# Kernel tuning notes

Measured on AMD Instinct MI355X. Metric: run time of the kernel, lower is better.

## Reference

```python
import jax, jax.numpy as jnp
import numpy as np

N_EMBD = 1024
N_HEAD = 16
HEAD_DIM = N_EMBD // N_HEAD  # 64
R = 8
D_STD = HEAD_DIM - R         # 56
BLOCK_SIZE = 2048
B, T = 2, 2048
NEG = -1e9


def setup_inputs() -> dict:
    key = jax.random.key(0)
    ks = jax.random.split(key, 8)
    x = jax.random.normal(ks[0], (B, T, N_EMBD), dtype=jnp.float32)
    Wqkv = jax.random.normal(ks[1], (3 * N_EMBD, N_EMBD), dtype=jnp.float32) * 0.02
    Wproj = jax.random.normal(ks[2], (N_EMBD, N_EMBD), dtype=jnp.float32) * 0.02
    W_recip = jax.random.normal(ks[3], (HEAD_DIM, R), dtype=jnp.float32) * 0.02
    # mixing weights must be positive (sqrt is taken); match init scale
    w_std = jnp.full((N_HEAD,), 0.5, dtype=jnp.float32)
    w_rec = jnp.full((N_HEAD,), 0.3, dtype=jnp.float32)  # > threshold -> all heads RA
    w_disc = jnp.full((N_HEAD,), 0.2, dtype=jnp.float32)
    d_bias = jax.random.normal(ks[4], (N_HEAD, BLOCK_SIZE), dtype=jnp.float32) * 0.02
    return {"x": x, "Wqkv": Wqkv, "Wproj": Wproj, "W_recip": W_recip,
            "w_std": w_std, "w_rec": w_rec, "w_disc": w_disc, "d_bias": d_bias}


def reference(x, Wqkv, Wproj, W_recip, w_std, w_rec, w_disc, d_bias):
    Bx, Tx, C = x.shape
    H, hd = N_HEAD, HEAD_DIM
    qkv = x @ Wqkv.T                                   # (B,T,3C)
    q, k, v = jnp.split(qkv, 3, axis=-1)
    def heads(t):
        return t.reshape(Bx, Tx, H, hd).transpose(0, 2, 1, 3)  # (B,H,T,hd)
    q, k, v = heads(q), heads(k), heads(v)
    q_low = jnp.einsum('bhtd,dr->bhtr', q, W_recip)    # (B,H,T,R)
    k_low = jnp.einsum('bhtd,dr->bhtr', k, W_recip)
    sw_std = jnp.sqrt(w_std)[None, :, None, None]
    sw_rec = jnp.sqrt(w_rec)[None, :, None, None]
    # cross augmentation: q side carries k_low, k side carries q_low
    q_aug = jnp.concatenate([sw_std * q[..., :D_STD], sw_rec * k_low], axis=-1)
    k_aug = jnp.concatenate([sw_std * k[..., :D_STD], sw_rec * q_low], axis=-1)
    scale = 1.0 / jnp.sqrt(jnp.asarray(hd, dtype=x.dtype))
    scores = jnp.einsum('bhqd,bhkd->bhqk', q_aug, k_aug) * scale
    # per-head learned bias over key positions, broadcast over queries
    bias = w_disc[None, :, None, None] * d_bias[:, :Tx][None, :, None, :]
    scores = scores + bias
    causal = jnp.tril(jnp.ones((Tx, Tx), dtype=bool))
    scores = jnp.where(causal[None, None], scores, NEG)
    attn = jax.nn.softmax(scores, axis=-1)
    out = jnp.einsum('bhqk,bhkd->bhqd', attn, v)       # (B,H,T,hd)
    out = out.transpose(0, 2, 1, 3).reshape(Bx, Tx, C)
    return out @ Wproj.T
```

## Files before the change

kernel.cpp:

```cpp
#include <hip/hip_runtime.h>
#include <math.h>

#define T_SEQ 2048
#define NH 16
#define HD 64
#define CEMB 1024
#define NEGINF -3.0e38f
#define LOG2E 1.4426950408889634f

typedef unsigned short ushort;
typedef unsigned int uint;
typedef __attribute__((ext_vector_type(8))) short short8;
typedef __attribute__((ext_vector_type(4))) float f32x4;

#if __has_builtin(__builtin_amdgcn_exp2f)
#define EXP2(x) __builtin_amdgcn_exp2f(x)
#else
#define EXP2(x) exp2f(x)
#endif

__device__ __forceinline__ float b2f(ushort h) {
    union { uint u; float f; } cv; cv.u = ((uint)h) << 16; return cv.f;
}
__device__ __forceinline__ ushort f2b(float f) {
    union { float f; uint u; } cv; cv.f = f;
    return (ushort)((cv.u + 0x7FFF + ((cv.u >> 16) & 1)) >> 16);
}
__device__ __forceinline__ ushort f2b_fast(float f) {
    union { float f; uint u; } cv; cv.f = f;
    return (ushort)((cv.u + 0x8000) >> 16);
}
__device__ __forceinline__ uint pack_bf16(float a, float b) {
    union { float f; uint u; } ua, ub; ua.f = a; ub.f = b;
    return __builtin_amdgcn_perm(ub.u + 0x8000u, ua.u + 0x8000u, 0x07060302u);
}
__device__ __forceinline__ void gl2lds16(const ushort* g, ushort* l) {
    __builtin_amdgcn_global_load_lds(
        (const __attribute__((address_space(1))) void*)g,
        (__attribute__((address_space(3))) void*)l, 16, 0, 0);
}

__global__ __launch_bounds__(256) void prep_kernel(
    const float* __restrict__ x, const float* __restrict__ Wqkv,
    const float* __restrict__ Wproj, const float* __restrict__ W_recip,
    const float* __restrict__ w_disc, const float* __restrict__ d_bias,
    ushort* __restrict__ xb, ushort* __restrict__ wqkvb,
    ushort* __restrict__ wprojb, float* __restrict__ bias_pre)
{
    const int bid = blockIdx.x;
    if (bid < 8192) {
        const float* src; ushort* dst; int off;
        if (bid < 4096)      { src = x;     dst = xb;     off = bid; }
        else if (bid < 7168) { src = Wqkv;  dst = wqkvb;  off = bid - 4096; }
        else                 { src = Wproj; dst = wprojb; off = bid - 7168; }
        const int i = (off * 256 + threadIdx.x) * 4;
        const float4 v = *(const float4*)&src[i];
        ushort4 o;
        o.x = f2b(v.x); o.y = f2b(v.y); o.z = f2b(v.z); o.w = f2b(v.w);
        *(ushort4*)&dst[i] = o;
        return;
    }
    if (bid >= 8224) {
        const int h = bid - 8224;
        const float wd = w_disc[h] * LOG2E;
        const int j = h * T_SEQ + threadIdx.x * 8;
        const float4 a = *(const float4*)&d_bias[j];
        const float4 c = *(const float4*)&d_bias[j + 4];
        float4 oa, oc;
        oa.x = a.x * wd; oa.y = a.y * wd; oa.z = a.z * wd; oa.w = a.w * wd;
        oc.x = c.x * wd; oc.y = c.y * wd; oc.z = c.z * wd; oc.w = c.w * wd;
        *(float4*)&bias_pre[j] = oa;
        *(float4*)&bias_pre[j + 4] = oc;
        return;
    }
    const int wb = bid - 8192;
    const int qk = wb >> 4, h = wb & 15;
    const int e0 = threadIdx.x * 4;
    f32x4 acc[8];
    #pragma unroll
    for (int r = 0; r < 8; ++r) acc[r] = (f32x4){0.f, 0.f, 0.f, 0.f};
    #pragma unroll 4
    for (int d = 0; d < 64; ++d) {
        const float4 xv = *(const float4*)&Wqkv[(size_t)(qk * 1024 + h * 64 + d) * 1024 + e0];
        #pragma unroll
        for (int r = 0; r < 8; ++r) {
            const float w = W_recip[d * 8 + r];
            acc[r][0] = fmaf(w, xv.x, acc[r][0]);
            acc[r][1] = fmaf(w, xv.y, acc[r][1]);
            acc[r][2] = fmaf(w, xv.z, acc[r][2]);
            acc[r][3] = fmaf(w, xv.w, acc[r][3]);
        }
    }
    #pragma unroll
    for (int r = 0; r < 8; ++r) {
        ushort4 o;
        o.x = f2b(acc[r][0]); o.y = f2b(acc[r][1]);
        o.z = f2b(acc[r][2]); o.w = f2b(acc[r][3]);
        *(ushort4*)&wqkvb[(size_t)(3072 + qk * 128 + h * 8 + r) * 1024 + e0] = o;
    }
}

#define GEMM_CORE(Aptr, Bptr, KDIM, SMEMN)                                     \
    __shared__ __align__(16) ushort SMEM[SMEMN];                               \
    ushort* const Asl = SMEM;                                                  \
    ushort* const Bsl = SMEM + 8192;                                           \
    const int row0 = blockIdx.x * 128;                                         \
    const int col0 = blockIdx.y * 128;                                         \
    const int tid = threadIdx.x;                                               \
    const int wave = tid >> 6, lane = tid & 63;                                \
    const int wm = wave >> 1, wn = wave & 1;                                   \
    const int quad = lane >> 4, lq = lane & 15;                                \
    const int l7 = lq & 7;                                                     \
    f32x4 acc[4][4];                                                           \
    _Pragma("unroll") for (int i = 0; i < 4; ++i)                              \
        _Pragma("unroll") for (int j = 0; j < 4; ++j)                          \
            acc[i][j] = (f32x4){0.f, 0.f, 0.f, 0.f};                           \
    for (int k0 = 0; k0 < (KDIM); k0 += 64) {                                  \
        _Pragma("unroll") for (int p = 0; p < 4; ++p) {                        \
            const int idx = p * 256 + tid;                                     \
            const int row = idx >> 3, slot = idx & 7;                          \
            const int kc = (slot ^ (row & 7)) << 3;                            \
            gl2lds16(&(Aptr)[(size_t)(row0 + row) * (KDIM) + k0 + kc], &Asl[idx * 8]); \
            gl2lds16(&(Bptr)[(size_t)(col0 + row) * (KDIM) + k0 + kc], &Bsl[idx * 8]); \
        }                                                                      \
        __syncthreads();                                                       \
        _Pragma("unroll") for (int ks = 0; ks < 2; ++ks) {                     \
            short8 af[4], bf[4];                                               \
            _Pragma("unroll") for (int i = 0; i < 4; ++i)                      \
                af[i] = *(const short8*)&Asl[(wm * 64 + i * 16 + lq) * 64 +    \
                                             (((ks * 4 + quad) ^ l7) << 3)];   \
            _Pragma("unroll") for (int j = 0; j < 4; ++j)                      \
                bf[j] = *(const short8*)&Bsl[(wn * 64 + j * 16 + lq) * 64 +    \
                                             (((ks * 4 + quad) ^ l7) << 3)];   \
            _Pragma("unroll") for (int i = 0; i < 4; ++i)                      \
                _Pragma("unroll") for (int j = 0; j < 4; ++j)                  \
                    acc[i][j] = __builtin_amdgcn_mfma_f32_16x16x32_bf16(       \
                        af[i], bf[j], acc[i][j], 0, 0, 0);                     \
        }                                                                      \
        __syncthreads();                                                       \
    }

__global__ __launch_bounds__(256, 4) void gemm_qkv_kernel(
    const ushort* __restrict__ A, const ushort* __restrict__ Bt,
    const float* __restrict__ w_std, const float* __restrict__ w_rec,
    ushort* __restrict__ qh, ushort* __restrict__ kh, ushort* __restrict__ vt)
{
    GEMM_CORE(A, Bt, 1024, 128 * 136)
    ushort* const Cs = SMEM;

    if (col0 >= 2048 && col0 < 3072) {
        #pragma unroll
        for (int j = 0; j < 4; ++j) {
            const int cc = col0 + wn * 64 + j * 16 + lq;
            const int h = (cc >> 6) & 15;
            const int d = cc & 63;
            #pragma unroll
            for (int i = 0; i < 4; ++i) {
                const int rr0 = row0 + wm * 64 + i * 16 + quad * 4;
                const int b = rr0 >> 11, t0 = rr0 & 2047;
                ushort4 pv;
                pv.x = f2b(acc[i][j][0]); pv.y = f2b(acc[i][j][1]);
                pv.z = f2b(acc[i][j][2]); pv.w = f2b(acc[i][j][3]);
                *(ushort4*)&vt[((((size_t)b * NH + h) * HD + d) * T_SEQ + t0)] = pv;
            }
        }
    } else if (col0 < 2048) {
        const bool isq = (col0 < 1024);
        #pragma unroll
        for (int j = 0; j < 4; ++j) {
            const int colc = wn * 64 + j * 16 + lq;
            const int h = ((col0 + colc) >> 6) & 15;
            const float sc = isq ? w_std[h] * (0.125f * LOG2E) : 1.0f;
            #pragma unroll
            for (int i = 0; i < 4; ++i)
                #pragma unroll
                for (int r = 0; r < 4; ++r)
                    Cs[(wm * 64 + i * 16 + quad * 4 + r) * 136 + colc] =
                        f2b(acc[i][j][r] * sc);
        }
        __syncthreads();
        ushort* dst = isq ? qh : kh;
        const int hbase = (col0 >> 6) & 15;
        #pragma unroll
        for (int rep = 0; rep < 8; ++rep) {
            const int id = rep * 256 + tid;
            const int row = id >> 4, chunk = id & 15;
            if ((chunk & 7) == 7) continue;
            const int h = hbase + (chunk >> 3);
            const int d = (chunk & 7) * 8;
            const int rr = row0 + row;
            const int b = rr >> 11, t = rr & 2047;
            const uint4 val = *(const uint4*)&Cs[row * 136 + chunk * 8];
            *(uint4*)&dst[((((size_t)b * NH + h) * T_SEQ + t) * HD + d)] = val;
        }
    } else {
        const bool isqlow = (col0 < 3200);
        #pragma unroll
        for (int j = 0; j < 4; ++j) {
            const int colc = wn * 64 + j * 16 + lq;
            const int h = colc >> 3;
            const float sc = isqlow ? 1.0f : w_rec[h] * (0.125f * LOG2E);
            #pragma unroll
            for (int i = 0; i < 4; ++i)
                #pragma unroll
                for (int r = 0; r < 4; ++r)
                    Cs[(wm * 64 + i * 16 + quad * 4 + r) * 136 + colc] =
                        f2b(acc[i][j][r] * sc);
        }
        __syncthreads();
        ushort* dst = isqlow ? kh : qh;
        #pragma unroll
        for (int rep = 0; rep < 8; ++rep) {
            const int id = rep * 256 + tid;
            const int row = id >> 4, h = id & 15;
            const int rr = row0 + row;
            const int b = rr >> 11, t = rr & 2047;
            const uint4 val = *(const uint4*)&Cs[row * 136 + h * 8];
            *(uint4*)&dst[((((size_t)b * NH + h) * T_SEQ + t) * HD + 56)] = val;
        }
    }
}

__global__ __launch_bounds__(256, 4) void gemm_proj_kernel(
    const ushort* __restrict__ A, const ushort* __restrict__ Bt,
    float* __restrict__ C)
{
    GEMM_CORE(A, Bt, 1024, 16384)
    #pragma unroll
    for (int i = 0; i < 4; ++i) {
        #pragma unroll
        for (int r = 0; r < 4; ++r) {
            const int rr = row0 + wm * 64 + i * 16 + quad * 4 + r;
            #pragma unroll
            for (int j = 0; j < 4; ++j) {
                const int cc = col0 + wn * 64 + j * 16 + lq;
                C[(size_t)rr * 1024 + cc] = acc[i][j][r];
            }
        }
    }
}

__global__ __launch_bounds__(256, 4) void attn_kernel(
    const ushort* __restrict__ qa, const ushort* __restrict__ ka,
    const ushort* __restrict__ vt, const float* __restrict__ bias_pre,
    ushort* __restrict__ out)
{
    __shared__ __align__(16) ushort Qs[64 * 64];
    __shared__ __align__(16) ushort KPs[128 * 64];
    __shared__ __align__(16) ushort Vs[64 * 128];
    const int bh = blockIdx.x;
    const int qt = 31 - blockIdx.y;
    const int h = bh & 15;
    const int b = bh >> 4;
    const int tid = threadIdx.x;
    const int wave = tid >> 6, lane = tid & 63;
    const int quad = lane >> 4, lq = lane & 15;
    const int l7 = lq & 7;
    const size_t base = (size_t)bh * T_SEQ * HD;

    #pragma unroll
    for (int rep = 0; rep < 2; ++rep) {
        const int idx = rep * 256 + tid;
        const int row = idx >> 3, slot = idx & 7;
        gl2lds16(&qa[base + (size_t)(qt * 64 + row) * 64 + ((slot ^ (row & 7)) << 3)],
                 &Qs[idx * 8]);
    }
    __syncthreads();
    short8 bq[2];
    #pragma unroll
    for (int ks = 0; ks < 2; ++ks)
        bq[ks] = *(const short8*)&Qs[(wave * 16 + lq) * 64 + (((ks * 4 + quad) ^ l7) << 3)];

    f32x4 o4[4];
    #pragma unroll
    for (int dt = 0; dt < 4; ++dt) o4[dt] = (f32x4){0.f, 0.f, 0.f, 0.f};
    float lsum = 0.f;
    const int qrow = qt * 64 + wave * 16 + lq;
    const int prow = (wave * 16 + lq) * 128;
    const int nchunks = (qt + 2) >> 1;
    const float* bias_h = &bias_pre[h * T_SEQ];

    for (int c = 0; c < nchunks; ++c) {
        const int k0 = c * 128;
        if (c) __syncthreads();
        #pragma unroll
        for (int rep = 0; rep < 4; ++rep) {
            const int idx = rep * 256 + tid;
            const int row = idx >> 3, slot = idx & 7;
            gl2lds16(&ka[base + (size_t)(k0 + row) * 64 + ((slot ^ (row & 7)) << 3)],
                     &KPs[idx * 8]);
        }
        #pragma unroll
        for (int rep = 0; rep < 4; ++rep) {
            const int idx = rep * 256 + tid;
            const int row = idx >> 4, slot = idx & 15;
            gl2lds16(&vt[base + (size_t)row * T_SEQ + k0 + ((slot ^ (row & 15)) << 3)],
                     &Vs[idx * 8]);
        }
        __syncthreads();

        f32x4 s4[8];
        #pragma unroll
        for (int nt = 0; nt < 8; ++nt)
            s4[nt] = *(const f32x4*)&bias_h[k0 + nt * 16 + quad * 4];
        #pragma unroll
        for (int ks = 0; ks < 2; ++ks)
            #pragma unroll
            for (int nt = 0; nt < 8; ++nt) {
                const short8 ak = *(const short8*)
                    &KPs[(nt * 16 + lq) * 64 + (((ks * 4 + quad) ^ l7) << 3)];
                s4[nt] = __builtin_amdgcn_mfma_f32_16x16x32_bf16(
                    ak, bq[ks], s4[nt], 0, 0, 0);
            }
        __syncthreads();

        const bool lastc = (c == nchunks - 1);
        #pragma unroll
        for (int nt = 0; nt < 8; ++nt) {
            f32x4 sv = s4[nt];
            if (lastc) {
                const int kb = k0 + nt * 16 + quad * 4;
                #pragma unroll
                for (int r = 0; r < 4; ++r)
                    if (kb + r > qrow) sv[r] = NEGINF;
            }
            const float p0 = EXP2(sv[0]), p1 = EXP2(sv[1]);
            const float p2 = EXP2(sv[2]), p3 = EXP2(sv[3]);
            lsum += (p0 + p1) + (p2 + p3);
            const int pcol = (nt * 16 + quad * 4) ^ (l7 << 3);
            uint2 pv; pv.x = pack_bf16(p0, p1); pv.y = pack_bf16(p2, p3);
            *(uint2*)&KPs[prow + pcol] = pv;
        }

        #pragma unroll
        for (int ks = 0; ks < 4; ++ks) {
            const short8 bp = *(const short8*)
                &KPs[prow + ((ks * 32 + quad * 8) ^ (l7 << 3))];
            #pragma unroll
            for (int dt = 0; dt < 4; ++dt) {
                const short8 av = *(const short8*)
                    &Vs[(dt * 16 + lq) * 128 + (((ks * 4 + quad) ^ lq) << 3)];
                o4[dt] = __builtin_amdgcn_mfma_f32_16x16x32_bf16(
                    av, bp, o4[dt], 0, 0, 0);
            }
        }
    }

    lsum += __shfl_xor(lsum, 16, 64);
    lsum += __shfl_xor(lsum, 32, 64);
    const float inv = 1.0f / lsum;
    const size_t obase = ((size_t)b * T_SEQ + qrow) * CEMB + h * HD;
    #pragma unroll
    for (int dt = 0; dt < 4; ++dt) {
        ushort4 ov;
        ov.x = f2b_fast(o4[dt][0] * inv);
        ov.y = f2b_fast(o4[dt][1] * inv);
        ov.z = f2b_fast(o4[dt][2] * inv);
        ov.w = f2b_fast(o4[dt][3] * inv);
        *(ushort4*)&out[obase + dt * 16 + quad * 4] = ov;
    }
}

extern "C" void kernel_launch(void* const* d_in, const int* in_sizes, int n_in,
                              void* d_out, int out_size, void* d_ws, size_t ws_size,
                              hipStream_t stream) {
    const float* x       = (const float*)d_in[0];
    const float* Wqkv    = (const float*)d_in[1];
    const float* Wproj   = (const float*)d_in[2];
    const float* W_recip = (const float*)d_in[3];
    const float* w_std   = (const float*)d_in[4];
    const float* w_rec   = (const float*)d_in[5];
    const float* w_disc  = (const float*)d_in[6];
    const float* d_bias  = (const float*)d_in[7];
    float* out = (float*)d_out;

    const size_t NX = (size_t)4096 * 1024;
    const size_t NWQKVX = (size_t)3328 * 1024;
    const size_t NWPROJ = (size_t)1024 * 1024;
    ushort* xb     = (ushort*)d_ws;
    ushort* wqkvb  = xb + NX;
    ushort* wprojb = wqkvb + NWQKVX;
    ushort* qh     = wprojb + NWPROJ;
    ushort* kh     = qh + NX;
    ushort* vt     = kh + NX;
    ushort* ao     = vt + NX;
    float*  bias_pre = (float*)(ao + NX);

    prep_kernel<<<8240, 256, 0, stream>>>(x, Wqkv, Wproj, W_recip, w_disc, d_bias,
                                          xb, wqkvb, wprojb, bias_pre);
    gemm_qkv_kernel<<<dim3(32, 26), 256, 0, stream>>>(xb, wqkvb, w_std, w_rec, qh, kh, vt);
    attn_kernel<<<dim3(32, 32), 256, 0, stream>>>(qh, kh, vt, bias_pre, ao);
    gemm_proj_kernel<<<dim3(32, 8), 256, 0, stream>>>(ao, wprojb, out);
}
```

Measured before the change: 191.8 us.

## Pair light and heavy causal query tiles per block, sharing K/V loads

Each attention block now handles two query tiles, qt and 31-qt, so causal work is balanced across blocks and each K/V chunk loaded into LDS serves both tiles. P gets its own LDS buffer so the barrier between score computation and the P writes can go, and the last diagonal chunk skips its empty half when the tile index is even. The grid is halved and launch bounds drop to 2 blocks per CU because of the extra registers and LDS, which lowers occupancy.

```diff
diff --git a/kernel.cpp b/kernel.cpp
--- a/kernel.cpp
+++ b/kernel.cpp
@@ -240,18 +240,54 @@
     }
 }
 
-__global__ __launch_bounds__(256, 4) void attn_kernel(
+#define TILE_COMPUTE(bq, o4, lsum, qrow, NTL) do {                            \
+    f32x4 s4[8];                                                              \
+    _Pragma("unroll") for (int nt = 0; nt < (NTL); ++nt)                      \
+        s4[nt] = *(const f32x4*)&bias_h[k0 + nt * 16 + quad * 4];             \
+    _Pragma("unroll") for (int ks = 0; ks < 2; ++ks)                          \
+        _Pragma("unroll") for (int nt = 0; nt < (NTL); ++nt) {                \
+            const short8 ak = *(const short8*)                                \
+                &Ks[(nt * 16 + lq) * 64 + (((ks * 4 + quad) ^ l7) << 3)];     \
+            s4[nt] = __builtin_amdgcn_mfma_f32_16x16x32_bf16(                 \
+                ak, (bq)[ks], s4[nt], 0, 0, 0);                               \
+        }                                                                     \
+    _Pragma("unroll") for (int nt = 0; nt < (NTL); ++nt) {                    \
+        f32x4 sv = s4[nt];                                                    \
+        const int kb = k0 + nt * 16 + quad * 4;                               \
+        _Pragma("unroll") for (int r = 0; r < 4; ++r)                         \
+            if (kb + r > (qrow)) sv[r] = NEGINF;                              \
+        const float p0 = EXP2(sv[0]), p1 = EXP2(sv[1]);                       \
+        const float p2 = EXP2(sv[2]), p3 = EXP2(sv[3]);                       \
+        (lsum) += (p0 + p1) + (p2 + p3);                                      \
+        const int pcol = (nt * 16 + quad * 4) ^ (l7 << 3);                    \
+        uint2 pv; pv.x = pack_bf16(p0, p1); pv.y = pack_bf16(p2, p3);         \
+        *(uint2*)&Ps[prow + pcol] = pv;                                       \
+    }                                                                         \
+    _Pragma("unroll") for (int ks = 0; ks < (NTL) / 2; ++ks) {                \
+        const short8 bp = *(const short8*)                                    \
+            &Ps[prow + ((ks * 32 + quad * 8) ^ (l7 << 3))];                   \
+        _Pragma("unroll") for (int dt = 0; dt < 4; ++dt) {                    \
+            const short8 av = *(const short8*)                                \
+                &Vs[(dt * 16 + lq) * 128 + (((ks * 4 + quad) ^ lq) << 3)];    \
+            (o4)[dt] = __builtin_amdgcn_mfma_f32_16x16x32_bf16(               \
+                av, bp, (o4)[dt], 0, 0, 0);                                   \
+        }                                                                     \
+    }                                                                         \
+} while (0)
+
+__global__ __launch_bounds__(256, 2) void attn_kernel(
     const ushort* __restrict__ qa, const ushort* __restrict__ ka,
     const ushort* __restrict__ vt, const float* __restrict__ bias_pre,
     ushort* __restrict__ out)
 {
-    __shared__ __align__(16) ushort Qs[64 * 64];
-    __shared__ __align__(16) ushort KPs[128 * 64];
+    __shared__ __align__(16) ushort Qs[2 * 64 * 64];
+    __shared__ __align__(16) ushort Ks[128 * 64];
+    __shared__ __align__(16) ushort Ps[64 * 128];
     __shared__ __align__(16) ushort Vs[64 * 128];
     const int bh = blockIdx.x;
-    const int qt = 31 - blockIdx.y;
-    const int h = bh & 15;
-    const int b = bh >> 4;
+    const int qtA = blockIdx.y;
+    const int qtB = 31 - blockIdx.y;
+    const int h = bh & 15, b = bh >> 4;
     const int tid = threadIdx.x;
     const int wave = tid >> 6, lane = tid & 63;
     const int quad = lane >> 4, lq = lane & 15;
@@ -262,25 +298,33 @@
     for (int rep = 0; rep < 2; ++rep) {
         const int idx = rep * 256 + tid;
         const int row = idx >> 3, slot = idx & 7;
-        gl2lds16(&qa[base + (size_t)(qt * 64 + row) * 64 + ((slot ^ (row & 7)) << 3)],
-                 &Qs[idx * 8]);
+        const int kc = (slot ^ (row & 7)) << 3;
+        gl2lds16(&qa[base + (size_t)(qtA * 64 + row) * 64 + kc], &Qs[idx * 8]);
+        gl2lds16(&qa[base + (size_t)(qtB * 64 + row) * 64 + kc], &Qs[4096 + idx * 8]);
     }
     __syncthreads();
-    short8 bq[2];
-    #pragma unroll
-    for (int ks = 0; ks < 2; ++ks)
-        bq[ks] = *(const short8*)&Qs[(wave * 16 + lq) * 64 + (((ks * 4 + quad) ^ l7) << 3)];
-
-    f32x4 o4[4];
-    #pragma unroll
-    for (int dt = 0; dt < 4; ++dt) o4[dt] = (f32x4){0.f, 0.f, 0.f, 0.f};
-    float lsum = 0.f;
-    const int qrow = qt * 64 + wave * 16 + lq;
+    short8 bqA[2], bqB[2];
+    #pragma unroll
+    for (int ks = 0; ks < 2; ++ks) {
+        const int off = (wave * 16 + lq) * 64 + (((ks * 4 + quad) ^ l7) << 3);
+        bqA[ks] = *(const short8*)&Qs[off];
+        bqB[ks] = *(const short8*)&Qs[4096 + off];
+    }
+
+    f32x4 o4A[4], o4B[4];
+    #pragma unroll
+    for (int dt = 0; dt < 4; ++dt) {
+        o4A[dt] = (f32x4){0.f, 0.f, 0.f, 0.f};
+        o4B[dt] = (f32x4){0.f, 0.f, 0.f, 0.f};
+    }
+    float lsumA = 0.f, lsumB = 0.f;
+    const int qrowA = qtA * 64 + wave * 16 + lq;
+    const int qrowB = qtB * 64 + wave * 16 + lq;
     const int prow = (wave * 16 + lq) * 128;
-    const int nchunks = (qt + 2) >> 1;
+    const int nA = (qtA + 2) >> 1, nB = (qtB + 2) >> 1;
     const float* bias_h = &bias_pre[h * T_SEQ];
 
-    for (int c = 0; c < nchunks; ++c) {
+    for (int c = 0; c < nB; ++c) {
         const int k0 = c * 128;
         if (c) __syncthreads();
         #pragma unroll
@@ -288,7 +332,7 @@
             const int idx = rep * 256 + tid;
             const int row = idx >> 3, slot = idx & 7;
             gl2lds16(&ka[base + (size_t)(k0 + row) * 64 + ((slot ^ (row & 7)) << 3)],
-                     &KPs[idx * 8]);
+                     &Ks[idx * 8]);
         }
         #pragma unroll
         for (int rep = 0; rep < 4; ++rep) {
@@ -299,65 +343,35 @@
         }
         __syncthreads();
 
-        f32x4 s4[8];
-        #pragma unroll
-        for (int nt = 0; nt < 8; ++nt)
-            s4[nt] = *(const f32x4*)&bias_h[k0 + nt * 16 + quad * 4];
-        #pragma unroll
-        for (int ks = 0; ks < 2; ++ks)
-            #pragma unroll
-            for (int nt = 0; nt < 8; ++nt) {
-                const short8 ak = *(const short8*)
-                    &KPs[(nt * 16 + lq) * 64 + (((ks * 4 + quad) ^ l7) << 3)];
-                s4[nt] = __builtin_amdgcn_mfma_f32_16x16x32_bf16(
-                    ak, bq[ks], s4[nt], 0, 0, 0);
-            }
-        __syncthreads();
-
-        const bool lastc = (c == nchunks - 1);
-        #pragma unroll
-        for (int nt = 0; nt < 8; ++nt) {
-            f32x4 sv = s4[nt];
-            if (lastc) {
-                const int kb = k0 + nt * 16 + quad * 4;
-                #pragma unroll
-                for (int r = 0; r < 4; ++r)
-                    if (kb + r > qrow) sv[r] = NEGINF;
-            }
-            const float p0 = EXP2(sv[0]), p1 = EXP2(sv[1]);
-            const float p2 = EXP2(sv[2]), p3 = EXP2(sv[3]);
-            lsum += (p0 + p1) + (p2 + p3);
-            const int pcol = (nt * 16 + quad * 4) ^ (l7 << 3);
-            uint2 pv; pv.x = pack_bf16(p0, p1); pv.y = pack_bf16(p2, p3);
-            *(uint2*)&KPs[prow + pcol] = pv;
-        }
-
-        #pragma unroll
-        for (int ks = 0; ks < 4; ++ks) {
-            const short8 bp = *(const short8*)
-                &KPs[prow + ((ks * 32 + quad * 8) ^ (l7 << 3))];
-            #pragma unroll
-            for (int dt = 0; dt < 4; ++dt) {
-                const short8 av = *(const short8*)
-                    &Vs[(dt * 16 + lq) * 128 + (((ks * 4 + quad) ^ lq) << 3)];
-                o4[dt] = __builtin_amdgcn_mfma_f32_16x16x32_bf16(
-                    av, bp, o4[dt], 0, 0, 0);
-            }
-        }
-    }
-
-    lsum += __shfl_xor(lsum, 16, 64);
-    lsum += __shfl_xor(lsum, 32, 64);
-    const float inv = 1.0f / lsum;
-    const size_t obase = ((size_t)b * T_SEQ + qrow) * CEMB + h * HD;
+        if (c == nB - 1 && !(qtB & 1)) TILE_COMPUTE(bqB, o4B, lsumB, qrowB, 4);
+        else                           TILE_COMPUTE(bqB, o4B, lsumB, qrowB, 8);
+        if (c < nA) {
+            if (c == nA - 1 && !(qtA & 1)) TILE_COMPUTE(bqA, o4A, lsumA, qrowA, 4);
+            else                           TILE_COMPUTE(bqA, o4A, lsumA, qrowA, 8);
+        }
+    }
+
+    lsumA += __shfl_xor(lsumA, 16, 64);
+    lsumA += __shfl_xor(lsumA, 32, 64);
+    lsumB += __shfl_xor(lsumB, 16, 64);
+    lsumB += __shfl_xor(lsumB, 32, 64);
+    const float invA = 1.0f / lsumA, invB = 1.0f / lsumB;
+    const size_t obaseA = ((size_t)b * T_SEQ + qrowA) * CEMB + h * HD;
+    const size_t obaseB = ((size_t)b * T_SEQ + qrowB) * CEMB + h * HD;
     #pragma unroll
     for (int dt = 0; dt < 4; ++dt) {
         ushort4 ov;
-        ov.x = f2b_fast(o4[dt][0] * inv);
-        ov.y = f2b_fast(o4[dt][1] * inv);
-        ov.z = f2b_fast(o4[dt][2] * inv);
-        ov.w = f2b_fast(o4[dt][3] * inv);
-        *(ushort4*)&out[obase + dt * 16 + quad * 4] = ov;
+        ov.x = f2b_fast(o4A[dt][0] * invA);
+        ov.y = f2b_fast(o4A[dt][1] * invA);
+        ov.z = f2b_fast(o4A[dt][2] * invA);
+        ov.w = f2b_fast(o4A[dt][3] * invA);
+        *(ushort4*)&out[obaseA + dt * 16 + quad * 4] = ov;
+        ushort4 ow;
+        ow.x = f2b_fast(o4B[dt][0] * invB);
+        ow.y = f2b_fast(o4B[dt][1] * invB);
+        ow.z = f2b_fast(o4B[dt][2] * invB);
+        ow.w = f2b_fast(o4B[dt][3] * invB);
+        *(ushort4*)&out[obaseB + dt * 16 + quad * 4] = ow;
     }
 }
 
@@ -389,6 +403,6 @@
     prep_kernel<<<8240, 256, 0, stream>>>(x, Wqkv, Wproj, W_recip, w_disc, d_bias,
                                           xb, wqkvb, wprojb, bias_pre);
     gemm_qkv_kernel<<<dim3(32, 26), 256, 0, stream>>>(xb, wqkvb, w_std, w_rec, qh, kh, vt);
-    attn_kernel<<<dim3(32, 32), 256, 0, stream>>>(qh, kh, vt, bias_pre, ao);
+    attn_kernel<<<dim3(32, 16), 256, 0, stream>>>(qh, kh, vt, bias_pre, ao);
     gemm_proj_kernel<<<dim3(32, 8), 256, 0, stream>>>(ao, wprojb, out);
 }
```

Result: no change. 190.7 us (-0.6%).

## Process 128 query rows per attention block to reuse K/V tiles

Applied to the files above, without the earlier changes.

The attention kernel now handles 128 query rows per block (32 per wave, two 16-row sub-tiles), so each K/V tile staged in shared memory feeds twice as many MFMAs, and a separate P buffer replaces the shared K/P buffer. Q fragments load straight from global memory, the causal mask now applies to every chunk, block order is remapped to interleave heavy and light query tiles, and s_setprio brackets the MFMA phases. The intent is to halve K/V global loads and LDS staging per unit of work. In exchange the kernel uses more registers and LDS (launch bounds drop to 2 blocks per CU) and launches fewer blocks. The QKV GEMM epilogue stride also changes from 136 to 144.

```diff
diff --git a/kernel.cpp b/kernel.cpp
--- a/kernel.cpp
+++ b/kernel.cpp
@@ -140,12 +140,13 @@
         __syncthreads();                                                       \
     }
 
+#define CSTR 144
 __global__ __launch_bounds__(256, 4) void gemm_qkv_kernel(
     const ushort* __restrict__ A, const ushort* __restrict__ Bt,
     const float* __restrict__ w_std, const float* __restrict__ w_rec,
     ushort* __restrict__ qh, ushort* __restrict__ kh, ushort* __restrict__ vt)
 {
-    GEMM_CORE(A, Bt, 1024, 128 * 136)
+    GEMM_CORE(A, Bt, 1024, 128 * CSTR)
     ushort* const Cs = SMEM;
 
     if (col0 >= 2048 && col0 < 3072) {
@@ -175,7 +176,7 @@
             for (int i = 0; i < 4; ++i)
                 #pragma unroll
                 for (int r = 0; r < 4; ++r)
-                    Cs[(wm * 64 + i * 16 + quad * 4 + r) * 136 + colc] =
+                    Cs[(wm * 64 + i * 16 + quad * 4 + r) * CSTR + colc] =
                         f2b(acc[i][j][r] * sc);
         }
         __syncthreads();
@@ -190,7 +191,7 @@
             const int d = (chunk & 7) * 8;
             const int rr = row0 + row;
             const int b = rr >> 11, t = rr & 2047;
-            const uint4 val = *(const uint4*)&Cs[row * 136 + chunk * 8];
+            const uint4 val = *(const uint4*)&Cs[row * CSTR + chunk * 8];
             *(uint4*)&dst[((((size_t)b * NH + h) * T_SEQ + t) * HD + d)] = val;
         }
     } else {
@@ -204,7 +205,7 @@
             for (int i = 0; i < 4; ++i)
                 #pragma unroll
                 for (int r = 0; r < 4; ++r)
-                    Cs[(wm * 64 + i * 16 + quad * 4 + r) * 136 + colc] =
+                    Cs[(wm * 64 + i * 16 + quad * 4 + r) * CSTR + colc] =
                         f2b(acc[i][j][r] * sc);
         }
         __syncthreads();
@@ -215,7 +216,7 @@
             const int row = id >> 4, h = id & 15;
             const int rr = row0 + row;
             const int b = rr >> 11, t = rr & 2047;
-            const uint4 val = *(const uint4*)&Cs[row * 136 + h * 8];
+            const uint4 val = *(const uint4*)&Cs[row * CSTR + h * 8];
             *(uint4*)&dst[((((size_t)b * NH + h) * T_SEQ + t) * HD + 56)] = val;
         }
     }
@@ -240,47 +241,64 @@
     }
 }
 
-__global__ __launch_bounds__(256, 4) void attn_kernel(
+#define SOFTMAX_G(sarr, qrow, lsum, prowX) do {                               \
+    _Pragma("unroll") for (int nt = 0; nt < 8; ++nt) {                        \
+        f32x4 sv = (sarr)[nt];                                                \
+        const int kb = k0 + nt * 16 + quad * 4;                               \
+        _Pragma("unroll") for (int r = 0; r < 4; ++r)                         \
+            if (kb + r > (qrow)) sv[r] = NEGINF;                              \
+        const float p0 = EXP2(sv[0]), p1 = EXP2(sv[1]);                       \
+        const float p2 = EXP2(sv[2]), p3 = EXP2(sv[3]);                       \
+        (lsum) += (p0 + p1) + (p2 + p3);                                      \
+        const int pcol = (nt * 16 + quad * 4) ^ (l7 << 3);                    \
+        uint2 pv; pv.x = pack_bf16(p0, p1); pv.y = pack_bf16(p2, p3);         \
+        *(uint2*)&Ps[(prowX) + pcol] = pv;                                    \
+    }                                                                         \
+} while (0)
+
+__global__ __launch_bounds__(256, 2) void attn_kernel(
     const ushort* __restrict__ qa, const ushort* __restrict__ ka,
     const ushort* __restrict__ vt, const float* __restrict__ bias_pre,
     ushort* __restrict__ out)
 {
-    __shared__ __align__(16) ushort Qs[64 * 64];
-    __shared__ __align__(16) ushort KPs[128 * 64];
+    __shared__ __align__(16) ushort Ks[128 * 64];
     __shared__ __align__(16) ushort Vs[64 * 128];
+    __shared__ __align__(16) ushort Ps[128 * 128];
     const int bh = blockIdx.x;
-    const int qt = 31 - blockIdx.y;
-    const int h = bh & 15;
-    const int b = bh >> 4;
+    const int yy = blockIdx.y;
+    const int qt = (yy < 8) ? (15 - yy) : (yy - 8);
+    const int h = bh & 15, b = bh >> 4;
     const int tid = threadIdx.x;
     const int wave = tid >> 6, lane = tid & 63;
     const int quad = lane >> 4, lq = lane & 15;
     const int l7 = lq & 7;
     const size_t base = (size_t)bh * T_SEQ * HD;
 
-    #pragma unroll
-    for (int rep = 0; rep < 2; ++rep) {
-        const int idx = rep * 256 + tid;
-        const int row = idx >> 3, slot = idx & 7;
-        gl2lds16(&qa[base + (size_t)(qt * 64 + row) * 64 + ((slot ^ (row & 7)) << 3)],
-                 &Qs[idx * 8]);
-    }
-    __syncthreads();
-    short8 bq[2];
-    #pragma unroll
-    for (int ks = 0; ks < 2; ++ks)
-        bq[ks] = *(const short8*)&Qs[(wave * 16 + lq) * 64 + (((ks * 4 + quad) ^ l7) << 3)];
-
-    f32x4 o4[4];
-    #pragma unroll
-    for (int dt = 0; dt < 4; ++dt) o4[dt] = (f32x4){0.f, 0.f, 0.f, 0.f};
-    float lsum = 0.f;
-    const int qrow = qt * 64 + wave * 16 + lq;
-    const int prow = (wave * 16 + lq) * 128;
-    const int nchunks = (qt + 2) >> 1;
+    const int row_base = qt * 128 + wave * 32;
+    const int qrow0 = row_base + lq;
+    const int qrow1 = row_base + 16 + lq;
+    const int prow0 = (wave * 32 + lq) * 128;
+    const int prow1 = prow0 + 16 * 128;
+    const int nc = qt + 1;
     const float* bias_h = &bias_pre[h * T_SEQ];
 
-    for (int c = 0; c < nchunks; ++c) {
+    short8 bq0[2], bq1[2];
+    #pragma unroll
+    for (int ks = 0; ks < 2; ++ks) {
+        const int dq = (ks * 4 + quad) * 8;
+        bq0[ks] = *(const short8*)&qa[base + (size_t)qrow0 * 64 + dq];
+        bq1[ks] = *(const short8*)&qa[base + (size_t)qrow1 * 64 + dq];
+    }
+
+    f32x4 o40[4], o41[4];
+    #pragma unroll
+    for (int dt = 0; dt < 4; ++dt) {
+        o40[dt] = (f32x4){0.f, 0.f, 0.f, 0.f};
+        o41[dt] = (f32x4){0.f, 0.f, 0.f, 0.f};
+    }
+    float lsum0 = 0.f, lsum1 = 0.f;
+
+    for (int c = 0; c < nc; ++c) {
         const int k0 = c * 128;
         if (c) __syncthreads();
         #pragma unroll
@@ -288,7 +306,7 @@
             const int idx = rep * 256 + tid;
             const int row = idx >> 3, slot = idx & 7;
             gl2lds16(&ka[base + (size_t)(k0 + row) * 64 + ((slot ^ (row & 7)) << 3)],
-                     &KPs[idx * 8]);
+                     &Ks[idx * 8]);
         }
         #pragma unroll
         for (int rep = 0; rep < 4; ++rep) {
@@ -299,65 +317,69 @@
         }
         __syncthreads();
 
-        f32x4 s4[8];
-        #pragma unroll
-        for (int nt = 0; nt < 8; ++nt)
-            s4[nt] = *(const f32x4*)&bias_h[k0 + nt * 16 + quad * 4];
+        f32x4 s0[8], s1[8];
+        #pragma unroll
+        for (int nt = 0; nt < 8; ++nt) {
+            const f32x4 bv = *(const f32x4*)&bias_h[k0 + nt * 16 + quad * 4];
+            s0[nt] = bv; s1[nt] = bv;
+        }
+        __builtin_amdgcn_s_setprio(1);
         #pragma unroll
         for (int ks = 0; ks < 2; ++ks)
             #pragma unroll
             for (int nt = 0; nt < 8; ++nt) {
                 const short8 ak = *(const short8*)
-                    &KPs[(nt * 16 + lq) * 64 + (((ks * 4 + quad) ^ l7) << 3)];
-                s4[nt] = __builtin_amdgcn_mfma_f32_16x16x32_bf16(
-                    ak, bq[ks], s4[nt], 0, 0, 0);
+                    &Ks[(nt * 16 + lq) * 64 + (((ks * 4 + quad) ^ l7) << 3)];
+                s0[nt] = __builtin_amdgcn_mfma_f32_16x16x32_bf16(
+                    ak, bq0[ks], s0[nt], 0, 0, 0);
+                s1[nt] = __builtin_amdgcn_mfma_f32_16x16x32_bf16(
+                    ak, bq1[ks], s1[nt], 0, 0, 0);
             }
-        __syncthreads();
-
-        const bool lastc = (c == nchunks - 1);
-        #pragma unroll
-        for (int nt = 0; nt < 8; ++nt) {
-            f32x4 sv = s4[nt];
-            if (lastc) {
-                const int kb = k0 + nt * 16 + quad * 4;
-                #pragma unroll
-                for (int r = 0; r < 4; ++r)
-                    if (kb + r > qrow) sv[r] = NEGINF;
-            }
-            const float p0 = EXP2(sv[0]), p1 = EXP2(sv[1]);
-            const float p2 = EXP2(sv[2]), p3 = EXP2(sv[3]);
-            lsum += (p0 + p1) + (p2 + p3);
-            const int pcol = (nt * 16 + quad * 4) ^ (l7 << 3);
-            uint2 pv; pv.x = pack_bf16(p0, p1); pv.y = pack_bf16(p2, p3);
-            *(uint2*)&KPs[prow + pcol] = pv;
-        }
-
+        __builtin_amdgcn_s_setprio(0);
+
+        SOFTMAX_G(s0, qrow0, lsum0, prow0);
+        SOFTMAX_G(s1, qrow1, lsum1, prow1);
+
+        __builtin_amdgcn_s_setprio(1);
         #pragma unroll
         for (int ks = 0; ks < 4; ++ks) {
-            const short8 bp = *(const short8*)
-                &KPs[prow + ((ks * 32 + quad * 8) ^ (l7 << 3))];
+            const int pofc = (ks * 32 + quad * 8) ^ (l7 << 3);
+            const short8 bp0 = *(const short8*)&Ps[prow0 + pofc];
+            const short8 bp1 = *(const short8*)&Ps[prow1 + pofc];
             #pragma unroll
             for (int dt = 0; dt < 4; ++dt) {
                 const short8 av = *(const short8*)
                     &Vs[(dt * 16 + lq) * 128 + (((ks * 4 + quad) ^ lq) << 3)];
-                o4[dt] = __builtin_amdgcn_mfma_f32_16x16x32_bf16(
-                    av, bp, o4[dt], 0, 0, 0);
+                o40[dt] = __builtin_amdgcn_mfma_f32_16x16x32_bf16(
+                    av, bp0, o40[dt], 0, 0, 0);
+                o41[dt] = __builtin_amdgcn_mfma_f32_16x16x32_bf16(
+                    av, bp1, o41[dt], 0, 0, 0);
             }
         }
-    }
-
-    lsum += __shfl_xor(lsum, 16, 64);
-    lsum += __shfl_xor(lsum, 32, 64);
-    const float inv = 1.0f / lsum;
-    const size_t obase = ((size_t)b * T_SEQ + qrow) * CEMB + h * HD;
+        __builtin_amdgcn_s_setprio(0);
+    }
+
+    lsum0 += __shfl_xor(lsum0, 16, 64);
+    lsum0 += __shfl_xor(lsum0, 32, 64);
+    lsum1 += __shfl_xor(lsum1, 16, 64);
+    lsum1 += __shfl_xor(lsum1, 32, 64);
+    const float inv0 = 1.0f / lsum0, inv1 = 1.0f / lsum1;
+    const size_t ob0 = ((size_t)b * T_SEQ + qrow0) * CEMB + h * HD;
+    const size_t ob1 = ((size_t)b * T_SEQ + qrow1) * CEMB + h * HD;
     #pragma unroll
     for (int dt = 0; dt < 4; ++dt) {
         ushort4 ov;
-        ov.x = f2b_fast(o4[dt][0] * inv);
-        ov.y = f2b_fast(o4[dt][1] * inv);
-        ov.z = f2b_fast(o4[dt][2] * inv);
-        ov.w = f2b_fast(o4[dt][3] * inv);
-        *(ushort4*)&out[obase + dt * 16 + quad * 4] = ov;
+        ov.x = f2b_fast(o40[dt][0] * inv0);
+        ov.y = f2b_fast(o40[dt][1] * inv0);
+        ov.z = f2b_fast(o40[dt][2] * inv0);
+        ov.w = f2b_fast(o40[dt][3] * inv0);
+        *(ushort4*)&out[ob0 + dt * 16 + quad * 4] = ov;
+        ushort4 ow;
+        ow.x = f2b_fast(o41[dt][0] * inv1);
+        ow.y = f2b_fast(o41[dt][1] * inv1);
+        ow.z = f2b_fast(o41[dt][2] * inv1);
+        ow.w = f2b_fast(o41[dt][3] * inv1);
+        *(ushort4*)&out[ob1 + dt * 16 + quad * 4] = ow;
     }
 }
 
@@ -389,6 +411,6 @@
     prep_kernel<<<8240, 256, 0, stream>>>(x, Wqkv, Wproj, W_recip, w_disc, d_bias,
                                           xb, wqkvb, wprojb, bias_pre);
     gemm_qkv_kernel<<<dim3(32, 26), 256, 0, stream>>>(xb, wqkvb, w_std, w_rec, qh, kh, vt);
-    attn_kernel<<<dim3(32, 32), 256, 0, stream>>>(qh, kh, vt, bias_pre, ao);
+    attn_kernel<<<dim3(32, 16), 256, 0, stream>>>(qh, kh, vt, bias_pre, ao);
     gemm_proj_kernel<<<dim3(32, 8), 256, 0, stream>>>(ao, wprojb, out);
 }
```

After: 200.1 us. 1.04x slower.
